# Kernel tuning notes

Measured on AMD Instinct MI355X. Metric: run time of the kernel, lower is better.

Reference implementation:

```python
import jax, jax.numpy as jnp
import numpy as np

N_AGENTS = 32
STATE_DIM = 512
LATENT = 16
H = 64  # attention_hidden_dim
N1 = N_AGENTS
N2 = N_AGENTS * (N_AGENTS - 1) // 2
NF = N1 + N2
B = 32768
# pairwise indices, same order as itertools.combinations(range(n), 2)
_PI, _PJ = np.triu_indices(N_AGENTS, k=1)
PI = jnp.asarray(_PI)
PJ = jnp.asarray(_PJ)


def setup_inputs() -> dict:
    key = jax.random.key(0)
    ks = jax.random.split(key, 24)
    s = 0.1  # small init scale (xavier gain 0.5)
    inp = {
        "agent_q_values": jax.random.normal(ks[0], (B, N_AGENTS), jnp.float32),
        "state": jax.random.normal(ks[1], (B, STATE_DIM), jnp.float32),
        "agent_semantics": jax.random.normal(ks[2], (B, N_AGENTS, LATENT), jnp.float32),
        # order-1 shape functions, stacked over N1 functions, weights in [in,out] layout
        "w1_1": jax.random.normal(ks[3], (N1, 1, 8), jnp.float32) * s,
        "b1_1": jnp.zeros((N1, 8), jnp.float32),
        "w2_1": jax.random.normal(ks[4], (N1, 8, 4), jnp.float32) * s,
        "b2_1": jnp.zeros((N1, 4), jnp.float32),
        "w3_1": jax.random.normal(ks[5], (N1, 4, 1), jnp.float32) * s,
        "b3_1": jnp.zeros((N1, 1), jnp.float32),
        # order-2 shape functions, stacked over N2 pairs
        "w1_2": jax.random.normal(ks[6], (N2, 2, 8), jnp.float32) * s,
        "b1_2": jnp.zeros((N2, 8), jnp.float32),
        "w2_2": jax.random.normal(ks[7], (N2, 8, 4), jnp.float32) * s,
        "b2_2": jnp.zeros((N2, 4), jnp.float32),
        "w3_2": jax.random.normal(ks[8], (N2, 4, 1), jnp.float32) * s,
        "b3_2": jnp.zeros((N2, 1), jnp.float32),
        # state encoder
        "ws_w": jax.random.normal(ks[9], (STATE_DIM, H), jnp.float32) * (1.0 / np.sqrt(STATE_DIM)),
        "ws_b": jnp.zeros((H,), jnp.float32),
        # semantic encoder
        "wz_w": jax.random.normal(ks[10], (LATENT * N_AGENTS, H), jnp.float32) * (1.0 / np.sqrt(LATENT * N_AGENTS)),
        "wz_b": jnp.zeros((H,), jnp.float32),
        # attention net
        "wa1_w": jax.random.normal(ks[11], (2 * H, H), jnp.float32) * (1.0 / np.sqrt(2 * H)),
        "wa1_b": jnp.zeros((H,), jnp.float32),
        "wa2_w": jax.random.normal(ks[12], (H, NF), jnp.float32) * (1.0 / np.sqrt(H)),
        "wa2_b": jnp.zeros((NF,), jnp.float32),
        # bias net
        "wb1_w": jax.random.normal(ks[13], (STATE_DIM, H), jnp.float32) * (1.0 / np.sqrt(STATE_DIM)),
        "wb1_b": jnp.zeros((H,), jnp.float32),
        "wb2_w": jax.random.normal(ks[14], (H, 1), jnp.float32) * (1.0 / np.sqrt(H)),
        "wb2_b": jnp.zeros((1,), jnp.float32),
    }
    return inp


def _shape_fns(x, w1, b1, w2, b2, w3, b3):
    # x: [B, N, D_in]; weights stacked over N functions; abs() on weights (monotonicity)
    h = jax.nn.elu(jnp.einsum("bnd,ndh->bnh", x, jnp.abs(w1)) + b1)   # [B,N,8]
    h = jax.nn.elu(jnp.einsum("bnh,nhk->bnk", h, jnp.abs(w2)) + b2)   # [B,N,4]
    f = jnp.einsum("bnk,nk->bn", h, jnp.abs(w3)[:, :, 0]) + b3[:, 0]  # [B,N]
    return f


def reference(agent_q_values, state, agent_semantics,
              w1_1, b1_1, w2_1, b2_1, w3_1, b3_1,
              w1_2, b1_2, w2_2, b2_2, w3_2, b3_2,
              ws_w, ws_b, wz_w, wz_b,
              wa1_w, wa1_b, wa2_w, wa2_b,
              wb1_w, wb1_b, wb2_w, wb2_b):
    q = agent_q_values  # [B, n_agents]
    # order-1 shape functions: input is scalar Q_i
    f1 = _shape_fns(q[:, :, None], w1_1, b1_1, w2_1, b2_1, w3_1, b3_1)   # [B, N1]
    # order-2 shape functions: input is [Q_i, Q_j] per pair
    q_pairs = jnp.stack([q[:, PI], q[:, PJ]], axis=-1)                    # [B, N2, 2]
    f2 = _shape_fns(q_pairs, w1_2, b1_2, w2_2, b2_2, w3_2, b3_2)          # [B, N2]
    shape_outputs = jnp.concatenate([f1, f2], axis=-1)                    # [B, NF]

    state_enc = jax.nn.relu(state @ ws_w + ws_b)                          # [B, H]
    sem_flat = agent_semantics.reshape(agent_semantics.shape[0], -1)      # [B, n*latent]
    sem_enc = jax.nn.relu(sem_flat @ wz_w + wz_b)                         # [B, H]
    combined = jnp.concatenate([state_enc, sem_enc], axis=-1)             # [B, 2H]
    logits = jax.nn.relu(combined @ wa1_w + wa1_b) @ wa2_w + wa2_b        # [B, NF]
    attention_weights = jax.nn.softmax(logits, axis=-1)

    weighted_sum = jnp.sum(attention_weights * shape_outputs, axis=-1, keepdims=True)
    bias = jax.nn.relu(state @ wb1_w + wb1_b) @ wb2_w + wb2_b             # [B, 1]
    q_total = weighted_sum + bias
    return (q_total, attention_weights, shape_outputs)
```

## Files before the change

kernel.cpp:

```cpp
#include <hip/hip_runtime.h>
#include <cstdint>
#include <cstddef>

#define NAG 32
#define N1C 32
#define N2C 496
#define NF 528
#define HD 64
#define SD 512

typedef __attribute__((ext_vector_type(8))) short bf16x8;
typedef __attribute__((ext_vector_type(4))) float f32x4;
#define MFMA16(a, b, c) __builtin_amdgcn_mfma_f32_16x16x32_bf16(a, b, c, 0, 0, 0)

__device__ __forceinline__ unsigned short f2bf(float f) {
    unsigned int u = __float_as_uint(f);
    u += 0x7fffu + ((u >> 16) & 1u);
    return (unsigned short)(u >> 16);
}
__device__ __forceinline__ unsigned int pack2(float a, float b) {
    return (unsigned int)f2bf(a) | ((unsigned int)f2bf(b) << 16);
}
__device__ __forceinline__ float elu_f(float x) {
    return x > 0.f ? x : (__expf(x) - 1.f);
}

#define OFF_WST   0
#define OFF_WB1T  32768
#define OFF_WZT   65536
#define OFF_WA1T  98304
#define OFF_WA2T  106496
#define PREP_TOT  140288

__global__ __launch_bounds__(256) void prep_kernel(
    const float* __restrict__ ws_w, const float* __restrict__ wb1_w,
    const float* __restrict__ wz_w, const float* __restrict__ wa1_w,
    const float* __restrict__ wa2_w, unsigned short* __restrict__ ws)
{
    int i = blockIdx.x * 256 + threadIdx.x;
    if (i >= PREP_TOT) return;
    float v;
    if (i < OFF_WB1T) {
        int j = i - OFF_WST; int n = j >> 9, k = j & 511;
        v = ws_w[k * 64 + n];
    } else if (i < OFF_WZT) {
        int j = i - OFF_WB1T; int n = j >> 9, k = j & 511;
        v = wb1_w[k * 64 + n];
    } else if (i < OFF_WA1T) {
        int j = i - OFF_WZT; int n = j >> 9, k = j & 511;
        v = wz_w[k * 64 + n];
    } else if (i < OFF_WA2T) {
        int j = i - OFF_WA1T; int n = j >> 7, k = j & 127;
        v = wa1_w[k * 64 + n];
    } else {
        int j = i - OFF_WA2T; int n = j >> 6, k = j & 63;
        v = wa2_w[k * NF + n];
    }
    ws[i] = f2bf(v);
}

#define SROWS 64
__global__ __launch_bounds__(576) void shape_kernel(
    const float* __restrict__ q,
    const float* __restrict__ w1_1, const float* __restrict__ b1_1,
    const float* __restrict__ w2_1, const float* __restrict__ b2_1,
    const float* __restrict__ w3_1, const float* __restrict__ b3_1,
    const float* __restrict__ w1_2, const float* __restrict__ b1_2,
    const float* __restrict__ w2_2, const float* __restrict__ b2_2,
    const float* __restrict__ w3_2, const float* __restrict__ b3_2,
    float* __restrict__ shape_out, int B)
{
    __shared__ float qs[SROWS][NAG];

    int tid = threadIdx.x;
    int f = tid;
    bool valid = f < NF;
    int fe = valid ? f : (NF - 1);

    float w1a[8], w1b[8], b1v[8], w2v[32], b2v[4], w3v[4], b3v;
    int pi, pj;
    if (fe < N1C) {
        int n = fe;
        pi = n; pj = n;
        #pragma unroll
        for (int k = 0; k < 8; k++) { w1a[k] = fabsf(w1_1[n*8+k]); w1b[k] = 0.f; b1v[k] = b1_1[n*8+k]; }
        #pragma unroll
        for (int t = 0; t < 32; t++) w2v[t] = fabsf(w2_1[n*32+t]);
        #pragma unroll
        for (int j = 0; j < 4; j++) { b2v[j] = b2_1[n*4+j]; w3v[j] = fabsf(w3_1[n*4+j]); }
        b3v = b3_1[n];
    } else {
        int n = fe - N1C;
        int p = n, i = 0, c = NAG - 1;
        while (p >= c) { p -= c; c--; i++; }
        pi = i; pj = i + 1 + p;
        #pragma unroll
        for (int k = 0; k < 8; k++) { w1a[k] = fabsf(w1_2[n*16+k]); w1b[k] = fabsf(w1_2[n*16+8+k]); b1v[k] = b1_2[n*8+k]; }
        #pragma unroll
        for (int t = 0; t < 32; t++) w2v[t] = fabsf(w2_2[n*32+t]);
        #pragma unroll
        for (int j = 0; j < 4; j++) { b2v[j] = b2_2[n*4+j]; w3v[j] = fabsf(w3_2[n*4+j]); }
        b3v = b3_2[n];
    }

    int row0 = blockIdx.x * SROWS;
    if (tid < 512) {
        float4 v = *(const float4*)&q[(size_t)row0 * NAG + tid * 4];
        *(float4*)&((float*)qs)[tid * 4] = v;
    }
    __syncthreads();

    #pragma unroll 4
    for (int rr = 0; rr < SROWS; rr++) {
        float qi = qs[rr][pi];
        float qj = qs[rr][pj];
        float h1[8];
        #pragma unroll
        for (int k = 0; k < 8; k++) h1[k] = elu_f(w1a[k]*qi + w1b[k]*qj + b1v[k]);
        float h2[4];
        #pragma unroll
        for (int j = 0; j < 4; j++) {
            float a = b2v[j];
            #pragma unroll
            for (int k = 0; k < 8; k++) a += h1[k] * w2v[k*4 + j];
            h2[j] = elu_f(a);
        }
        float fv = b3v;
        #pragma unroll
        for (int j = 0; j < 4; j++) fv += h2[j] * w3v[j];
        if (valid) shape_out[(size_t)(row0 + rr) * NF + f] = fv;
    }
}

#define RB 64
#define KH 256
#define SAP 264

__global__ __launch_bounds__(256, 2) void enc_mfma(
    const float* __restrict__ state,
    const float* __restrict__ sem,
    const unsigned short* __restrict__ wsbuf,
    const float* __restrict__ ws_b, const float* __restrict__ wz_b,
    const float* __restrict__ wa1_b, const float* __restrict__ wa2_b,
    const float* __restrict__ wb1_b, const float* __restrict__ wb2_w,
    const float* __restrict__ wb2_b,
    const float* __restrict__ shape_out,
    float* __restrict__ q_total,
    float* __restrict__ attn_out)
{
    __shared__ unsigned short sA[RB][SAP];
    __shared__ unsigned short sComb[RB][136];
    __shared__ unsigned short sH[RB][72];

    const unsigned short* wsT  = wsbuf + OFF_WST;
    const unsigned short* wb1T = wsbuf + OFF_WB1T;
    const unsigned short* wzT  = wsbuf + OFF_WZT;
    const unsigned short* wa1T = wsbuf + OFF_WA1T;
    const unsigned short* wa2T = wsbuf + OFF_WA2T;

    int tid  = threadIdx.x;
    int lane = tid & 63;
    int w    = tid >> 6;
    int col  = lane & 15;
    int quad = lane >> 4;
    int r0   = blockIdx.x * RB;
    int rowt = w * 16;

    const unsigned short* bS0 = wsT  + col * SD + quad * 8;
    const unsigned short* bB0 = wb1T + col * SD + quad * 8;
    const unsigned short* bZ0 = wzT  + col * SD + quad * 8;

    f32x4 accS[4], accB[4], accZ[4];
    #pragma unroll
    for (int ct = 0; ct < 4; ct++) {
        accS[ct] = (f32x4){0.f,0.f,0.f,0.f};
        accB[ct] = (f32x4){0.f,0.f,0.f,0.f};
        accZ[ct] = (f32x4){0.f,0.f,0.f,0.f};
    }

    #pragma unroll 1
    for (int h = 0; h < 2; h++) {
        int c0 = h * KH;
        #pragma unroll
        for (int b = 0; b < 2; b++) {
            float4 v[8];
            #pragma unroll
            for (int i = 0; i < 8; i++)
                v[i] = *(const float4*)&state[(size_t)(r0 + rowt + b*8 + i) * SD + c0 + lane * 4];
            #pragma unroll
            for (int i = 0; i < 8; i++) {
                uint2 p; p.x = pack2(v[i].x, v[i].y); p.y = pack2(v[i].z, v[i].w);
                *(uint2*)&sA[rowt + b*8 + i][lane * 4] = p;
            }
        }
        #pragma unroll
        for (int ks = 0; ks < 8; ks++) {
            bf16x8 a = *(const bf16x8*)&sA[rowt + col][ks * 32 + quad * 8];
            int wof = c0 + ks * 32;
            #pragma unroll
            for (int ct = 0; ct < 4; ct++) {
                bf16x8 bS = *(const bf16x8*)(bS0 + ct * 16 * SD + wof);
                bf16x8 bB = *(const bf16x8*)(bB0 + ct * 16 * SD + wof);
                accS[ct] = MFMA16(a, bS, accS[ct]);
                accB[ct] = MFMA16(a, bB, accB[ct]);
            }
        }
    }

    #pragma unroll 1
    for (int h = 0; h < 2; h++) {
        int c0 = h * KH;
        #pragma unroll
        for (int b = 0; b < 2; b++) {
            float4 v[8];
            #pragma unroll
            for (int i = 0; i < 8; i++)
                v[i] = *(const float4*)&sem[(size_t)(r0 + rowt + b*8 + i) * SD + c0 + lane * 4];
            #pragma unroll
            for (int i = 0; i < 8; i++) {
                uint2 p; p.x = pack2(v[i].x, v[i].y); p.y = pack2(v[i].z, v[i].w);
                *(uint2*)&sA[rowt + b*8 + i][lane * 4] = p;
            }
        }
        #pragma unroll
        for (int ks = 0; ks < 8; ks++) {
            bf16x8 a = *(const bf16x8*)&sA[rowt + col][ks * 32 + quad * 8];
            int wof = c0 + ks * 32;
            #pragma unroll
            for (int ct = 0; ct < 4; ct++) {
                bf16x8 bZ = *(const bf16x8*)(bZ0 + ct * 16 * SD + wof);
                accZ[ct] = MFMA16(a, bZ, accZ[ct]);
            }
        }
    }

    #pragma unroll
    for (int ct = 0; ct < 4; ct++) {
        float bs = ws_b[ct * 16 + col];
        float bz = wz_b[ct * 16 + col];
        #pragma unroll
        for (int reg = 0; reg < 4; reg++) {
            int rr = rowt + quad * 4 + reg;
            sComb[rr][ct * 16 + col]      = f2bf(fmaxf(accS[ct][reg] + bs, 0.f));
            sComb[rr][64 + ct * 16 + col] = f2bf(fmaxf(accZ[ct][reg] + bz, 0.f));
        }
    }

    float qbv[4];
    #pragma unroll
    for (int reg = 0; reg < 4; reg++) {
        float p = 0.f;
        #pragma unroll
        for (int ct = 0; ct < 4; ct++)
            p += fmaxf(accB[ct][reg] + wb1_b[ct * 16 + col], 0.f) * wb2_w[ct * 16 + col];
        #pragma unroll
        for (int m = 1; m < 16; m <<= 1) p += __shfl_xor(p, m, 64);
        qbv[reg] = p;
    }

    f32x4 accH[4];
    #pragma unroll
    for (int ct = 0; ct < 4; ct++) accH[ct] = (f32x4){0.f,0.f,0.f,0.f};
    #pragma unroll
    for (int ks = 0; ks < 4; ks++) {
        bf16x8 a = *(const bf16x8*)&sComb[rowt + col][ks * 32 + quad * 8];
        #pragma unroll
        for (int ct = 0; ct < 4; ct++) {
            bf16x8 b = *(const bf16x8*)&wa1T[(ct * 16 + col) * 128 + ks * 32 + quad * 8];
            accH[ct] = MFMA16(a, b, accH[ct]);
        }
    }
    #pragma unroll
    for (int ct = 0; ct < 4; ct++) {
        float bh = wa1_b[ct * 16 + col];
        #pragma unroll
        for (int reg = 0; reg < 4; reg++)
            sH[rowt + quad * 4 + reg][ct * 16 + col] = f2bf(fmaxf(accH[ct][reg] + bh, 0.f));
    }

    bf16x8 ha0 = *(const bf16x8*)&sH[rowt + col][quad * 8];
    bf16x8 ha1 = *(const bf16x8*)&sH[rowt + col][32 + quad * 8];

    float sAcc[4] = {0.f,0.f,0.f,0.f};
    float wAcc[4] = {0.f,0.f,0.f,0.f};
    for (int nt = 0; nt < 33; nt++) {
        f32x4 acc = (f32x4){0.f,0.f,0.f,0.f};
        const unsigned short* wp = &wa2T[(nt * 16 + col) * 64 + quad * 8];
        acc = MFMA16(ha0, *(const bf16x8*)wp, acc);
        acc = MFMA16(ha1, *(const bf16x8*)(wp + 32), acc);
        float lb = wa2_b[nt * 16 + col];
        #pragma unroll
        for (int reg = 0; reg < 4; reg++) {
            float e = __expf(acc[reg] + lb);
            sAcc[reg] += e;
            wAcc[reg] += e * shape_out[(size_t)(r0 + rowt + quad * 4 + reg) * NF + nt * 16 + col];
        }
    }
    float inv[4];
    #pragma unroll
    for (int reg = 0; reg < 4; reg++) {
        float s = sAcc[reg], ww = wAcc[reg];
        #pragma unroll
        for (int m = 1; m < 16; m <<= 1) { s += __shfl_xor(s, m, 64); ww += __shfl_xor(ww, m, 64); }
        inv[reg] = 1.f / s;
        if (col == 0)
            q_total[r0 + rowt + quad * 4 + reg] = ww * inv[reg] + qbv[reg] + wb2_b[0];
    }

    for (int nt = 0; nt < 33; nt++) {
        f32x4 acc = (f32x4){0.f,0.f,0.f,0.f};
        const unsigned short* wp = &wa2T[(nt * 16 + col) * 64 + quad * 8];
        acc = MFMA16(ha0, *(const bf16x8*)wp, acc);
        acc = MFMA16(ha1, *(const bf16x8*)(wp + 32), acc);
        float lb = wa2_b[nt * 16 + col];
        #pragma unroll
        for (int reg = 0; reg < 4; reg++) {
            float e = __expf(acc[reg] + lb);
            attn_out[(size_t)(r0 + rowt + quad * 4 + reg) * NF + nt * 16 + col] = e * inv[reg];
        }
    }
}

extern "C" void kernel_launch(void* const* d_in, const int* in_sizes, int n_in,
                              void* d_out, int out_size, void* d_ws, size_t ws_size,
                              hipStream_t stream) {
    const float* q     = (const float*)d_in[0];
    const float* state = (const float*)d_in[1];
    const float* sem   = (const float*)d_in[2];
    const float* w1_1  = (const float*)d_in[3];
    const float* b1_1  = (const float*)d_in[4];
    const float* w2_1  = (const float*)d_in[5];
    const float* b2_1  = (const float*)d_in[6];
    const float* w3_1  = (const float*)d_in[7];
    const float* b3_1  = (const float*)d_in[8];
    const float* w1_2  = (const float*)d_in[9];
    const float* b1_2  = (const float*)d_in[10];
    const float* w2_2  = (const float*)d_in[11];
    const float* b2_2  = (const float*)d_in[12];
    const float* w3_2  = (const float*)d_in[13];
    const float* b3_2  = (const float*)d_in[14];
    const float* ws_w  = (const float*)d_in[15];
    const float* ws_b  = (const float*)d_in[16];
    const float* wz_w  = (const float*)d_in[17];
    const float* wz_b  = (const float*)d_in[18];
    const float* wa1_w = (const float*)d_in[19];
    const float* wa1_b = (const float*)d_in[20];
    const float* wa2_w = (const float*)d_in[21];
    const float* wa2_b = (const float*)d_in[22];
    const float* wb1_w = (const float*)d_in[23];
    const float* wb1_b = (const float*)d_in[24];
    const float* wb2_w = (const float*)d_in[25];
    const float* wb2_b = (const float*)d_in[26];

    int B = in_sizes[0] / NAG;

    float* out_q    = (float*)d_out;
    float* out_attn = out_q + B;
    float* out_shp  = out_attn + (size_t)B * NF;

    unsigned short* wsbuf = (unsigned short*)d_ws;

    prep_kernel<<<(PREP_TOT + 255) / 256, 256, 0, stream>>>(
        ws_w, wb1_w, wz_w, wa1_w, wa2_w, wsbuf);

    shape_kernel<<<B / SROWS, 576, 0, stream>>>(q,
        w1_1, b1_1, w2_1, b2_1, w3_1, b3_1,
        w1_2, b1_2, w2_2, b2_2, w3_2, b3_2,
        out_shp, B);

    enc_mfma<<<B / RB, 256, 0, stream>>>(state, sem, wsbuf,
        ws_b, wz_b, wa1_b, wa2_b, wb1_b, wb2_w, wb2_b,
        out_shp, out_q, out_attn);
}
```

Baseline: 405.3 us.

## Fuse shape-function evaluation into the attention kernel, removing shape_out reread

Shape-function evaluation moves out of its own kernel and into the softmax loop of enc_mfma. Each lane computes the shape value for its (row, feature) pair from per-feature weights that prep_kernel packs into the workspace, writes it out, and uses it directly in the weighted sum. This removes the shape_kernel launch and the reread of the B×528 shape_out array. The cost is extra ALU work and weight loads inside the softmax loop, and heavier register pressure in a kernel launched with two blocks per CU. The state and semantic load batches also shrink from 8 rows to 4 per step.

Result: slower. 733.4 us (+80.9%).

```diff
diff --git a/kernel.cpp b/kernel.cpp
--- a/kernel.cpp
+++ b/kernel.cpp
@@ -31,105 +31,65 @@
 #define OFF_WA1T  98304
 #define OFF_WA2T  106496
 #define PREP_TOT  140288
+#define WFS       68
 
 __global__ __launch_bounds__(256) void prep_kernel(
     const float* __restrict__ ws_w, const float* __restrict__ wb1_w,
     const float* __restrict__ wz_w, const float* __restrict__ wa1_w,
-    const float* __restrict__ wa2_w, unsigned short* __restrict__ ws)
-{
-    int i = blockIdx.x * 256 + threadIdx.x;
-    if (i >= PREP_TOT) return;
-    float v;
-    if (i < OFF_WB1T) {
-        int j = i - OFF_WST; int n = j >> 9, k = j & 511;
-        v = ws_w[k * 64 + n];
-    } else if (i < OFF_WZT) {
-        int j = i - OFF_WB1T; int n = j >> 9, k = j & 511;
-        v = wb1_w[k * 64 + n];
-    } else if (i < OFF_WA1T) {
-        int j = i - OFF_WZT; int n = j >> 9, k = j & 511;
-        v = wz_w[k * 64 + n];
-    } else if (i < OFF_WA2T) {
-        int j = i - OFF_WA1T; int n = j >> 7, k = j & 127;
-        v = wa1_w[k * 64 + n];
-    } else {
-        int j = i - OFF_WA2T; int n = j >> 6, k = j & 63;
-        v = wa2_w[k * NF + n];
-    }
-    ws[i] = f2bf(v);
-}
-
-#define SROWS 64
-__global__ __launch_bounds__(576) void shape_kernel(
-    const float* __restrict__ q,
+    const float* __restrict__ wa2_w,
     const float* __restrict__ w1_1, const float* __restrict__ b1_1,
     const float* __restrict__ w2_1, const float* __restrict__ b2_1,
     const float* __restrict__ w3_1, const float* __restrict__ b3_1,
     const float* __restrict__ w1_2, const float* __restrict__ b1_2,
     const float* __restrict__ w2_2, const float* __restrict__ b2_2,
     const float* __restrict__ w3_2, const float* __restrict__ b3_2,
-    float* __restrict__ shape_out, int B)
+    unsigned short* __restrict__ ws)
 {
-    __shared__ float qs[SROWS][NAG];
-
-    int tid = threadIdx.x;
-    int f = tid;
-    bool valid = f < NF;
-    int fe = valid ? f : (NF - 1);
-
-    float w1a[8], w1b[8], b1v[8], w2v[32], b2v[4], w3v[4], b3v;
+    int i = blockIdx.x * 256 + threadIdx.x;
+    if (i < PREP_TOT) {
+        float v;
+        if (i < OFF_WB1T) {
+            int j = i - OFF_WST; int n = j >> 9, k = j & 511;
+            v = ws_w[k * 64 + n];
+        } else if (i < OFF_WZT) {
+            int j = i - OFF_WB1T; int n = j >> 9, k = j & 511;
+            v = wb1_w[k * 64 + n];
+        } else if (i < OFF_WA1T) {
+            int j = i - OFF_WZT; int n = j >> 9, k = j & 511;
+            v = wz_w[k * 64 + n];
+        } else if (i < OFF_WA2T) {
+            int j = i - OFF_WA1T; int n = j >> 7, k = j & 127;
+            v = wa1_w[k * 64 + n];
+        } else {
+            int j = i - OFF_WA2T; int n = j >> 6, k = j & 63;
+            v = wa2_w[k * NF + n];
+        }
+        ws[i] = f2bf(v);
+        return;
+    }
+    int f = i - PREP_TOT;
+    if (f >= NF) return;
+    float* wf = (float*)(ws + PREP_TOT) + (size_t)f * WFS;
     int pi, pj;
-    if (fe < N1C) {
-        int n = fe;
-        pi = n; pj = n;
-        #pragma unroll
-        for (int k = 0; k < 8; k++) { w1a[k] = fabsf(w1_1[n*8+k]); w1b[k] = 0.f; b1v[k] = b1_1[n*8+k]; }
-        #pragma unroll
-        for (int t = 0; t < 32; t++) w2v[t] = fabsf(w2_1[n*32+t]);
-        #pragma unroll
-        for (int j = 0; j < 4; j++) { b2v[j] = b2_1[n*4+j]; w3v[j] = fabsf(w3_1[n*4+j]); }
-        b3v = b3_1[n];
+    if (f < N1C) {
+        int n = f; pi = n; pj = n;
+        for (int k = 0; k < 8; k++) { wf[k] = fabsf(w1_1[n*8+k]); wf[8+k] = 0.f; wf[16+k] = b1_1[n*8+k]; }
+        for (int t = 0; t < 32; t++) wf[24+t] = fabsf(w2_1[n*32+t]);
+        for (int j = 0; j < 4; j++) { wf[56+j] = b2_1[n*4+j]; wf[60+j] = fabsf(w3_1[n*4+j]); }
+        wf[64] = b3_1[n];
     } else {
-        int n = fe - N1C;
-        int p = n, i = 0, c = NAG - 1;
-        while (p >= c) { p -= c; c--; i++; }
-        pi = i; pj = i + 1 + p;
-        #pragma unroll
-        for (int k = 0; k < 8; k++) { w1a[k] = fabsf(w1_2[n*16+k]); w1b[k] = fabsf(w1_2[n*16+8+k]); b1v[k] = b1_2[n*8+k]; }
-        #pragma unroll
-        for (int t = 0; t < 32; t++) w2v[t] = fabsf(w2_2[n*32+t]);
-        #pragma unroll
-        for (int j = 0; j < 4; j++) { b2v[j] = b2_2[n*4+j]; w3v[j] = fabsf(w3_2[n*4+j]); }
-        b3v = b3_2[n];
-    }
-
-    int row0 = blockIdx.x * SROWS;
-    if (tid < 512) {
-        float4 v = *(const float4*)&q[(size_t)row0 * NAG + tid * 4];
-        *(float4*)&((float*)qs)[tid * 4] = v;
-    }
-    __syncthreads();
-
-    #pragma unroll 4
-    for (int rr = 0; rr < SROWS; rr++) {
-        float qi = qs[rr][pi];
-        float qj = qs[rr][pj];
-        float h1[8];
-        #pragma unroll
-        for (int k = 0; k < 8; k++) h1[k] = elu_f(w1a[k]*qi + w1b[k]*qj + b1v[k]);
-        float h2[4];
-        #pragma unroll
-        for (int j = 0; j < 4; j++) {
-            float a = b2v[j];
-            #pragma unroll
-            for (int k = 0; k < 8; k++) a += h1[k] * w2v[k*4 + j];
-            h2[j] = elu_f(a);
-        }
-        float fv = b3v;
-        #pragma unroll
-        for (int j = 0; j < 4; j++) fv += h2[j] * w3v[j];
-        if (valid) shape_out[(size_t)(row0 + rr) * NF + f] = fv;
-    }
+        int n = f - N1C;
+        int p = n, ii = 0, c = NAG - 1;
+        while (p >= c) { p -= c; c--; ii++; }
+        pi = ii; pj = ii + 1 + p;
+        for (int k = 0; k < 8; k++) { wf[k] = fabsf(w1_2[n*16+k]); wf[8+k] = fabsf(w1_2[n*16+8+k]); wf[16+k] = b1_2[n*8+k]; }
+        for (int t = 0; t < 32; t++) wf[24+t] = fabsf(w2_2[n*32+t]);
+        for (int j = 0; j < 4; j++) { wf[56+j] = b2_2[n*4+j]; wf[60+j] = fabsf(w3_2[n*4+j]); }
+        wf[64] = b3_2[n];
+    }
+    wf[65] = __int_as_float(pi);
+    wf[66] = __int_as_float(pj);
+    wf[67] = 0.f;
 }
 
 #define RB 64
@@ -137,20 +97,23 @@
 #define SAP 264
 
 __global__ __launch_bounds__(256, 2) void enc_mfma(
+    const float* __restrict__ q,
     const float* __restrict__ state,
     const float* __restrict__ sem,
     const unsigned short* __restrict__ wsbuf,
+    const float* __restrict__ wfbuf,
     const float* __restrict__ ws_b, const float* __restrict__ wz_b,
     const float* __restrict__ wa1_b, const float* __restrict__ wa2_b,
     const float* __restrict__ wb1_b, const float* __restrict__ wb2_w,
     const float* __restrict__ wb2_b,
-    const float* __restrict__ shape_out,
+    float* __restrict__ shape_out,
     float* __restrict__ q_total,
     float* __restrict__ attn_out)
 {
     __shared__ unsigned short sA[RB][SAP];
     __shared__ unsigned short sComb[RB][136];
     __shared__ unsigned short sH[RB][72];
+    __shared__ float qs[RB][36];
 
     const unsigned short* wsT  = wsbuf + OFF_WST;
     const unsigned short* wb1T = wsbuf + OFF_WB1T;
@@ -166,6 +129,16 @@
     int r0   = blockIdx.x * RB;
     int rowt = w * 16;
 
+    #pragma unroll
+    for (int b = 0; b < 2; b++) {
+        int idx = b * 64 + lane;
+        int qr  = idx >> 3;
+        int qc  = (idx & 7) * 4;
+        float4 v = *(const float4*)&q[(size_t)(r0 + rowt + qr) * NAG + qc];
+        qs[rowt + qr][qc + 0] = v.x; qs[rowt + qr][qc + 1] = v.y;
+        qs[rowt + qr][qc + 2] = v.z; qs[rowt + qr][qc + 3] = v.w;
+    }
+
     const unsigned short* bS0 = wsT  + col * SD + quad * 8;
     const unsigned short* bB0 = wb1T + col * SD + quad * 8;
     const unsigned short* bZ0 = wzT  + col * SD + quad * 8;
@@ -182,15 +155,15 @@
     for (int h = 0; h < 2; h++) {
         int c0 = h * KH;
         #pragma unroll
-        for (int b = 0; b < 2; b++) {
-            float4 v[8];
-            #pragma unroll
-            for (int i = 0; i < 8; i++)
-                v[i] = *(const float4*)&state[(size_t)(r0 + rowt + b*8 + i) * SD + c0 + lane * 4];
-            #pragma unroll
-            for (int i = 0; i < 8; i++) {
+        for (int b = 0; b < 4; b++) {
+            float4 v[4];
+            #pragma unroll
+            for (int i = 0; i < 4; i++)
+                v[i] = *(const float4*)&state[(size_t)(r0 + rowt + b*4 + i) * SD + c0 + lane * 4];
+            #pragma unroll
+            for (int i = 0; i < 4; i++) {
                 uint2 p; p.x = pack2(v[i].x, v[i].y); p.y = pack2(v[i].z, v[i].w);
-                *(uint2*)&sA[rowt + b*8 + i][lane * 4] = p;
+                *(uint2*)&sA[rowt + b*4 + i][lane * 4] = p;
             }
         }
         #pragma unroll
@@ -211,15 +184,15 @@
     for (int h = 0; h < 2; h++) {
         int c0 = h * KH;
         #pragma unroll
-        for (int b = 0; b < 2; b++) {
-            float4 v[8];
-            #pragma unroll
-            for (int i = 0; i < 8; i++)
-                v[i] = *(const float4*)&sem[(size_t)(r0 + rowt + b*8 + i) * SD + c0 + lane * 4];
-            #pragma unroll
-            for (int i = 0; i < 8; i++) {
+        for (int b = 0; b < 4; b++) {
+            float4 v[4];
+            #pragma unroll
+            for (int i = 0; i < 4; i++)
+                v[i] = *(const float4*)&sem[(size_t)(r0 + rowt + b*4 + i) * SD + c0 + lane * 4];
+            #pragma unroll
+            for (int i = 0; i < 4; i++) {
                 uint2 p; p.x = pack2(v[i].x, v[i].y); p.y = pack2(v[i].z, v[i].w);
-                *(uint2*)&sA[rowt + b*8 + i][lane * 4] = p;
+                *(uint2*)&sA[rowt + b*4 + i][lane * 4] = p;
             }
         }
         #pragma unroll
@@ -283,17 +256,41 @@
 
     float sAcc[4] = {0.f,0.f,0.f,0.f};
     float wAcc[4] = {0.f,0.f,0.f,0.f};
+    #pragma unroll 1
     for (int nt = 0; nt < 33; nt++) {
         f32x4 acc = (f32x4){0.f,0.f,0.f,0.f};
         const unsigned short* wp = &wa2T[(nt * 16 + col) * 64 + quad * 8];
         acc = MFMA16(ha0, *(const bf16x8*)wp, acc);
         acc = MFMA16(ha1, *(const bf16x8*)(wp + 32), acc);
         float lb = wa2_b[nt * 16 + col];
+
+        const float* wf = wfbuf + (size_t)(nt * 16 + col) * WFS;
+        int pi = __float_as_int(wf[65]);
+        int pj = __float_as_int(wf[66]);
         #pragma unroll
         for (int reg = 0; reg < 4; reg++) {
+            int rr = rowt + quad * 4 + reg;
+            float qi = qs[rr][pi];
+            float qj = qs[rr][pj];
+            float h1[8];
+            #pragma unroll
+            for (int k = 0; k < 8; k++)
+                h1[k] = elu_f(wf[k] * qi + wf[8 + k] * qj + wf[16 + k]);
+            float h2[4];
+            #pragma unroll
+            for (int j = 0; j < 4; j++) {
+                float a = wf[56 + j];
+                #pragma unroll
+                for (int k = 0; k < 8; k++) a += h1[k] * wf[24 + k * 4 + j];
+                h2[j] = elu_f(a);
+            }
+            float fv = wf[64];
+            #pragma unroll
+            for (int j = 0; j < 4; j++) fv += h2[j] * wf[60 + j];
+            shape_out[(size_t)(r0 + rr) * NF + nt * 16 + col] = fv;
             float e = __expf(acc[reg] + lb);
             sAcc[reg] += e;
-            wAcc[reg] += e * shape_out[(size_t)(r0 + rowt + quad * 4 + reg) * NF + nt * 16 + col];
+            wAcc[reg] += e * fv;
         }
     }
     float inv[4];
@@ -359,16 +356,15 @@
     float* out_shp  = out_attn + (size_t)B * NF;
 
     unsigned short* wsbuf = (unsigned short*)d_ws;
-
-    prep_kernel<<<(PREP_TOT + 255) / 256, 256, 0, stream>>>(
-        ws_w, wb1_w, wz_w, wa1_w, wa2_w, wsbuf);
-
-    shape_kernel<<<B / SROWS, 576, 0, stream>>>(q,
+    const float* wfbuf = (const float*)(wsbuf + PREP_TOT);
+
+    prep_kernel<<<(PREP_TOT + NF + 255) / 256, 256, 0, stream>>>(
+        ws_w, wb1_w, wz_w, wa1_w, wa2_w,
         w1_1, b1_1, w2_1, b2_1, w3_1, b3_1,
         w1_2, b1_2, w2_2, b2_2, w3_2, b3_2,
-        out_shp, B);
-
-    enc_mfma<<<B / RB, 256, 0, stream>>>(state, sem, wsbuf,
+        wsbuf);
+
+    enc_mfma<<<B / RB, 256, 0, stream>>>(q, state, sem, wsbuf, wfbuf,
         ws_b, wz_b, wa1_b, wa2_b, wb1_b, wb2_w, wb2_b,
         out_shp, out_q, out_attn);
 }
```
